# Performance work log

Hardware: AMD Instinct MI355X
Metric: run time of the kernel (lower is better)

## Reference

```python
import jax, jax.numpy as jnp
import numpy as np

B, S, D = 4, 2048, 1024

def setup_inputs() -> dict:
    key = jax.random.key(0)
    ks = jax.random.split(key, 7)
    sc = 1.0 / np.sqrt(D)
    return {
        "x": jax.random.normal(ks[0], (B, S, D), dtype=jnp.float32),
        "Wq": jax.random.normal(ks[1], (D, D), dtype=jnp.float32) * sc,
        "bq": jax.random.normal(ks[2], (D,), dtype=jnp.float32) * 0.01,
        "Wk": jax.random.normal(ks[3], (D, D), dtype=jnp.float32) * sc,
        "bk": jax.random.normal(ks[4], (D,), dtype=jnp.float32) * 0.01,
        "Wv": jax.random.normal(ks[5], (D, D), dtype=jnp.float32) * sc,
        "bv": jax.random.normal(ks[6], (D,), dtype=jnp.float32) * 0.01,
    }

def reference(x, Wq, bq, Wk, bk, Wv, bv):
    # q, k, v: [B, S, D] projections (torch Linear: x @ W^T + b; here W stored as [in, out])
    q = jnp.einsum("bsd,df->bsf", x, Wq) + bq
    k = jnp.einsum("bsd,df->bsf", x, Wk) + bk
    v = jnp.einsum("bsd,df->bsf", x, Wv) + bv
    dim = x.shape[-1]
    # scores: [B, S, S], scaled by sqrt(full d_model) as in the source
    scores = jnp.einsum("bqd,bkd->bqk", q, k) / jnp.sqrt(jnp.float32(dim)).astype(x.dtype)
    attn = jax.nn.softmax(scores, axis=-1)
    return jnp.einsum("bqk,bkd->bqd", attn, v)
```

## Files before the change

### kernel.cpp

```cpp
#include <hip/hip_runtime.h>
#include <hip/hip_bf16.h>

typedef __attribute__((ext_vector_type(8))) short bf16x8;
typedef __attribute__((ext_vector_type(4))) float f32x4;
typedef unsigned short u16;

__device__ __forceinline__ u16 f2bf(float f) {
  unsigned int u = __builtin_bit_cast(unsigned int, f);
  u += 0x7fffu + ((u >> 16) & 1u);
  return (u16)(u >> 16);
}
__device__ __forceinline__ float bf2f(unsigned int h) {
  unsigned int u = h << 16;
  return __builtin_bit_cast(float, u);
}

__device__ __forceinline__ void gload_lds16(const void* g, void* l) {
  __builtin_amdgcn_global_load_lds(
      (const __attribute__((address_space(1))) void*)g,
      (__attribute__((address_space(3))) void*)l, 16, 0, 0);
}

#define BAR() __builtin_amdgcn_s_barrier()
#define VMC(N) asm volatile("s_waitcnt vmcnt(%0)" ::"n"(N) : "memory")

template <int EPI>
__global__ __launch_bounds__(512, 2) void gemm2t(
    const u16* __restrict__ Abase, const u16* __restrict__ Btbase,
    const float* __restrict__ p0, float* __restrict__ p1,
    const float* __restrict__ p2, void* __restrict__ out0,
    void* __restrict__ out1, int Kd, int ldc, long long sAz, long long sBz,
    long long sCz) {
  constexpr int ASZ = 16384;
  constexpr int BSZ = 32768;
  constexpr int BBASE = 2 * ASZ;
  __shared__ char lds[2 * ASZ + 3 * BSZ];

  const int tid = threadIdx.x;
  const int w = tid >> 6, l = tid & 63;
  const int wr = w >> 2, wc = w & 3;
  const int lq = l >> 4, lr = l & 15;
  const int bm = blockIdx.y * 128, bn = blockIdx.x * 256;
  const int z = blockIdx.z;
  const u16* A = Abase + (size_t)z * sAz;
  const u16* Bt = Btbase + (size_t)z * sBz;
  const int NT = Kd >> 6;

  const int kbp = ((tid & 7) ^ ((tid >> 3) & 7)) * 8;
  const int drow = tid >> 3;
  const u16* gA[2];
  const u16* gB[4];
#pragma unroll
  for (int u = 0; u < 2; ++u)
    gA[u] = A + (size_t)(bm + u * 64 + drow) * Kd + kbp;
#pragma unroll
  for (int u = 0; u < 4; ++u)
    gB[u] = Bt + (size_t)(bn + u * 64 + drow) * Kd + kbp;

  auto stageA = [&](int kt) {
    char* d = lds + (kt & 1) * ASZ + tid * 16;
#pragma unroll
    for (int u = 0; u < 2; ++u) gload_lds16(gA[u] + kt * 64, d + u * 8192);
  };
  auto stageB = [&](int kt) {
    char* d = lds + BBASE + (kt % 3) * BSZ + tid * 16;
#pragma unroll
    for (int u = 0; u < 4; ++u) gload_lds16(gB[u] + kt * 64, d + u * 8192);
  };

  const int rA = wr * 64 + lr;
  const int rB0 = wc * 64 + lr;
  int aoff[2];
#pragma unroll
  for (int kh = 0; kh < 2; ++kh)
    aoff[kh] = rA * 128 + (((kh * 4 + lq) ^ (rA & 7)) << 4);

  f32x4 acc[4][2][2] = {};
  bf16x8 a[2][4];
  bf16x8 bb[2][2][2];

  auto rdA = [&](int kt) {
    const char* p = lds + (kt & 1) * ASZ;
#pragma unroll
    for (int kh = 0; kh < 2; ++kh)
#pragma unroll
      for (int mf = 0; mf < 4; ++mf)
        a[kh][mf] = *(const bf16x8*)(p + aoff[kh] + mf * 2048);
  };
  auto rdB = [&](int kt) {
    const char* p = lds + BBASE + (kt % 3) * BSZ;
#pragma unroll
    for (int nh = 0; nh < 2; ++nh) {
      const int rB = rB0 + nh * 32;
#pragma unroll
      for (int kh = 0; kh < 2; ++kh) {
        const int o = rB * 128 + (((kh * 4 + lq) ^ (rB & 7)) << 4);
#pragma unroll
        for (int nf = 0; nf < 2; ++nf)
          bb[nh][kh][nf] = *(const bf16x8*)(p + o + nf * 2048);
      }
    }
  };
  auto mma = [&](int kh) {
    __builtin_amdgcn_s_setprio(1);
#pragma unroll
    for (int nh = 0; nh < 2; ++nh)
#pragma unroll
      for (int mf = 0; mf < 4; ++mf)
#pragma unroll
        for (int nf = 0; nf < 2; ++nf)
          acc[mf][nh][nf] = __builtin_amdgcn_mfma_f32_16x16x32_bf16(
              a[kh][mf], bb[nh][kh][nf], acc[mf][nh][nf], 0, 0, 0);
    __builtin_amdgcn_s_setprio(0);
  };

  stageB(0);
  stageA(0);
  stageB(1);
  stageA(1);
  VMC(6);
  BAR();

  for (int t = 0; t < NT; ++t) {
    rdA(t);
    rdB(t);
    if (t + 2 < NT) stageB(t + 2);
    BAR();
    mma(0);
    if (t + 2 < NT) VMC(4); else VMC(0);
    BAR();
    if (t + 2 < NT) stageA(t + 2);
    mma(1);
  }

  if constexpr (EPI == 4) {
    constexpr float K2 = 0.045084834f;
    u16* C = (u16*)out0 + (size_t)z * sCz;
    const float* cc = p0 + z * 2048;
    float* rs = p1 + z * 2048;
    float psum[4][4] = {};
#pragma unroll
    for (int nh = 0; nh < 2; ++nh)
#pragma unroll
      for (int nf = 0; nf < 2; ++nf) {
        const int col = bn + wc * 64 + nh * 32 + nf * 16 + lr;
        const float cj2 = cc[col];
#pragma unroll
        for (int mf = 0; mf < 4; ++mf) {
          const int row = bm + wr * 64 + mf * 16 + lq * 4;
#pragma unroll
          for (int e = 0; e < 4; ++e) {
            const float pv = exp2f(fmaf(acc[mf][nh][nf][e], K2, cj2));
            C[(size_t)(row + e) * ldc + col] = f2bf(pv);
            psum[mf][e] += pv;
          }
        }
      }
#pragma unroll
    for (int off = 1; off <= 8; off <<= 1)
#pragma unroll
      for (int mf = 0; mf < 4; ++mf)
#pragma unroll
        for (int e = 0; e < 4; ++e)
          psum[mf][e] += __shfl_xor(psum[mf][e], off, 64);
    if (lr == 0) {
#pragma unroll
      for (int mf = 0; mf < 4; ++mf)
#pragma unroll
        for (int e = 0; e < 4; ++e)
          atomicAdd(&rs[bm + wr * 64 + mf * 16 + lq * 4 + e], psum[mf][e]);
    }
  } else if constexpr (EPI == 5) {
    float* C = (float*)out0 + (size_t)z * sCz;
    const float* rs = p1 + z * 2048;
#pragma unroll
    for (int nh = 0; nh < 2; ++nh)
#pragma unroll
      for (int nf = 0; nf < 2; ++nf) {
        const int col = bn + wc * 64 + nh * 32 + nf * 16 + lr;
#pragma unroll
        for (int mf = 0; mf < 4; ++mf) {
          const int row = bm + wr * 64 + mf * 16 + lq * 4;
#pragma unroll
          for (int e = 0; e < 4; ++e)
            C[(size_t)(row + e) * ldc + col] =
                acc[mf][nh][nf][e] / rs[row + e];
        }
      }
  } else {
    const int mat = bn >> 10;
    u16* T = (u16*)out0;
    u16* V = (u16*)out1;
#pragma unroll
    for (int nh = 0; nh < 2; ++nh)
#pragma unroll
      for (int nf = 0; nf < 2; ++nf) {
        const int oc = (bn + wc * 64 + nh * 32 + nf * 16 + lr) & 1023;
        if (mat == 0) {
#pragma unroll
          for (int mf = 0; mf < 4; ++mf) {
            const int row = bm + wr * 64 + mf * 16 + lq * 4;
#pragma unroll
            for (int e = 0; e < 4; ++e)
              T[(size_t)(row + e) * 1024 + oc] = f2bf(acc[mf][nh][nf][e]);
          }
        } else {
          const float bb2 = p2[oc];
#pragma unroll
          for (int mf = 0; mf < 4; ++mf) {
            const int row = bm + wr * 64 + mf * 16 + lq * 4;
            const int bz = row >> 11, sdx = row & 2047;
            ushort4 pk;
            pk.x = f2bf(acc[mf][nh][nf][0] + bb2);
            pk.y = f2bf(acc[mf][nh][nf][1] + bb2);
            pk.z = f2bf(acc[mf][nh][nf][2] + bb2);
            pk.w = f2bf(acc[mf][nh][nf][3] + bb2);
            *(ushort4*)&V[((size_t)bz * 1024 + oc) * 2048 + sdx] = pk;
          }
        }
      }
  }
}

__global__ __launch_bounds__(256) void gemmM(
    const u16* __restrict__ Abase, const u16* __restrict__ Btbase,
    float* __restrict__ out0, int Kd, int Kext, int ldc, long long sAz,
    long long sBz, long long sCz) {
  constexpr int ASZ = 16384;
  constexpr int BSZ = 16384;
  constexpr int BBASE = 2 * ASZ;
  __shared__ char lds[2 * ASZ + 3 * BSZ];

  const int tid = threadIdx.x;
  const int w = tid >> 6, l = tid & 63;
  const int wr = w >> 1, wc = w & 1;
  const int lq = l >> 4, lr = l & 15;
  const int bm = blockIdx.y * 128, bn = blockIdx.x * 128;
  const int z = blockIdx.z;
  const u16* A = Abase + (size_t)z * sAz;
  const u16* Bt = Btbase + (size_t)z * sBz;
  const int NT = Kext >> 6;

  const int kbp = ((tid & 7) ^ ((tid >> 3) & 7)) * 8;
  const int drow = tid >> 3;
  const u16* gA[4];
  const u16* gB[4];
#pragma unroll
  for (int u = 0; u < 4; ++u) {
    gA[u] = A + (size_t)(bm + u * 32 + drow) * Kd + kbp;
    gB[u] = Bt + (size_t)(bn + u * 32 + drow) * Kd + kbp;
  }

  auto stageA = [&](int kt) {
    char* d = lds + (kt & 1) * ASZ + tid * 16;
#pragma unroll
    for (int u = 0; u < 4; ++u) gload_lds16(gA[u] + kt * 64, d + u * 4096);
  };
  auto stageB = [&](int kt) {
    char* d = lds + BBASE + (kt % 3) * BSZ + tid * 16;
#pragma unroll
    for (int u = 0; u < 4; ++u) gload_lds16(gB[u] + kt * 64, d + u * 4096);
  };

  const int rA = wr * 64 + lr;
  const int rB0 = wc * 64 + lr;
  int aoff[2];
#pragma unroll
  for (int kh = 0; kh < 2; ++kh)
    aoff[kh] = rA * 128 + (((kh * 4 + lq) ^ (rA & 7)) << 4);

  f32x4 acc[4][2][2] = {};
  bf16x8 a[2][4];
  bf16x8 bb[2][2][2];

  auto rdA = [&](int kt) {
    const char* p = lds + (kt & 1) * ASZ;
#pragma unroll
    for (int kh = 0; kh < 2; ++kh)
#pragma unroll
      for (int mf = 0; mf < 4; ++mf)
        a[kh][mf] = *(const bf16x8*)(p + aoff[kh] + mf * 2048);
  };
  auto rdB = [&](int kt) {
    const char* p = lds + BBASE + (kt % 3) * BSZ;
#pragma unroll
    for (int nh = 0; nh < 2; ++nh) {
      const int rB = rB0 + nh * 32;
#pragma unroll
      for (int kh = 0; kh < 2; ++kh) {
        const int o = rB * 128 + (((kh * 4 + lq) ^ (rB & 7)) << 4);
#pragma unroll
        for (int nf = 0; nf < 2; ++nf)
          bb[nh][kh][nf] = *(const bf16x8*)(p + o + nf * 2048);
      }
    }
  };
  auto mma = [&](int kh) {
#pragma unroll
    for (int nh = 0; nh < 2; ++nh)
#pragma unroll
      for (int mf = 0; mf < 4; ++mf)
#pragma unroll
        for (int nf = 0; nf < 2; ++nf)
          acc[mf][nh][nf] = __builtin_amdgcn_mfma_f32_16x16x32_bf16(
              a[kh][mf], bb[nh][kh][nf], acc[mf][nh][nf], 0, 0, 0);
  };

  stageB(0);
  stageA(0);
  stageB(1);
  stageA(1);
  VMC(8);
  BAR();

  for (int t = 0; t < NT; ++t) {
    rdA(t);
    rdB(t);
    if (t + 2 < NT) stageB(t + 2);
    BAR();
    mma(0);
    if (t + 2 < NT) VMC(4); else VMC(0);
    BAR();
    if (t + 2 < NT) stageA(t + 2);
    mma(1);
  }

  float* C = out0 + (size_t)z * sCz;
#pragma unroll
  for (int nh = 0; nh < 2; ++nh)
#pragma unroll
    for (int nf = 0; nf < 2; ++nf) {
      const int col = bn + wc * 64 + nh * 32 + nf * 16 + lr;
#pragma unroll
      for (int mf = 0; mf < 4; ++mf) {
        const int row = bm + wr * 64 + mf * 16 + lq * 4;
#pragma unroll
        for (int e = 0; e < 4; ++e)
          C[(size_t)(row + e) * ldc + col] = acc[mf][nh][nf][e];
      }
    }
}

__global__ __launch_bounds__(256) void prep(
    const float* __restrict__ x, const float* __restrict__ Wq,
    const float* __restrict__ Wk, const float* __restrict__ Wv,
    const float* __restrict__ bq, u16* __restrict__ xb,
    u16* __restrict__ Wqb, u16* __restrict__ Wkb, u16* __restrict__ WtTV,
    float* __restrict__ vvec) {
  const int bid = blockIdx.x;
  const int tid = threadIdx.x;
  if (bid < 8192) {
    const int i = bid * 256 + tid;
    const float4 v = ((const float4*)x)[i];
    ushort4 o;
    o.x = f2bf(v.x);
    o.y = f2bf(v.y);
    o.z = f2bf(v.z);
    o.w = f2bf(v.w);
    ((ushort4*)xb)[i] = o;
  } else if (bid < 11264) {
    const int b = bid - 8192;
    const int zz = b >> 10, t2 = b & 1023;
    const int k0 = (t2 >> 5) * 32, n0 = (t2 & 31) * 32;
    const int tx = tid & 31, ty0 = tid >> 5;
    if (zz == 2) {
      __shared__ float s[32][33];
#pragma unroll
      for (int r = 0; r < 4; ++r) {
        const int row = ty0 + 8 * r;
        s[row][tx] = Wv[(size_t)(k0 + row) * 1024 + n0 + tx];
      }
      __syncthreads();
#pragma unroll
      for (int r = 0; r < 4; ++r) {
        const int row = ty0 + 8 * r;
        WtTV[1048576 + (size_t)(n0 + row) * 1024 + k0 + tx] =
            f2bf(s[tx][row]);
      }
    } else {
      const float* W = zz ? Wk : Wq;
      u16* O = zz ? Wkb : Wqb;
#pragma unroll
      for (int r = 0; r < 4; ++r) {
        const size_t i = (size_t)(k0 + ty0 + 8 * r) * 1024 + n0 + tx;
        O[i] = f2bf(W[i]);
      }
    }
  } else {
    const int d = bid - 11264;
    const float4 wv = ((const float4*)(Wk + (size_t)d * 1024))[tid];
    const float4 bv = ((const float4*)bq)[tid];
    float p = wv.x * bv.x + wv.y * bv.y + wv.z * bv.z + wv.w * bv.w;
#pragma unroll
    for (int o = 32; o; o >>= 1) p += __shfl_xor(p, o, 64);
    __shared__ float red[4];
    if ((tid & 63) == 0) red[tid >> 6] = p;
    __syncthreads();
    if (tid == 0) vvec[d] = red[0] + red[1] + red[2] + red[3];
  }
}

__global__ __launch_bounds__(256) void mcast(const float* __restrict__ Mf,
                                             u16* __restrict__ Mt) {
  const int i = blockIdx.x * 256 + threadIdx.x;
  const float4 a = ((const float4*)Mf)[i];
  const float4 b = ((const float4*)(Mf + 1048576))[i];
  const float4 c = ((const float4*)(Mf + 2097152))[i];
  const float4 d = ((const float4*)(Mf + 3145728))[i];
  ushort4 o;
  o.x = f2bf(a.x + b.x + c.x + d.x);
  o.y = f2bf(a.y + b.y + c.y + d.y);
  o.z = f2bf(a.z + b.z + c.z + d.z);
  o.w = f2bf(a.w + b.w + c.w + d.w);
  ((ushort4*)Mt)[i] = o;
}

__global__ __launch_bounds__(256) void cker(const u16* __restrict__ xb,
                                            const float* __restrict__ v,
                                            float* __restrict__ c,
                                            float* __restrict__ rowsum) {
  if (blockIdx.x < 32) rowsum[blockIdx.x * 256 + threadIdx.x] = 0.f;
  const int j = blockIdx.x * 8 + (threadIdx.x >> 5);
  const int lane = threadIdx.x & 31;
  const u16* xr = xb + (size_t)j * 1024;
  float p = 0.f;
#pragma unroll
  for (int k = 0; k < 4; ++k) {
    const int g = k * 32 + lane;
    const uint4 u = ((const uint4*)xr)[g];
    const float4 v0 = ((const float4*)v)[g * 2];
    const float4 v1 = ((const float4*)v)[g * 2 + 1];
    p += bf2f(u.x & 0xffffu) * v0.x + bf2f(u.x >> 16) * v0.y +
         bf2f(u.y & 0xffffu) * v0.z + bf2f(u.y >> 16) * v0.w +
         bf2f(u.z & 0xffffu) * v1.x + bf2f(u.z >> 16) * v1.y +
         bf2f(u.w & 0xffffu) * v1.z + bf2f(u.w >> 16) * v1.w;
  }
#pragma unroll
  for (int o = 16; o; o >>= 1) p += __shfl_xor(p, o, 64);
  if (lane == 0) c[j] = p * 0.045084834f;
}

extern "C" void kernel_launch(void* const* d_in, const int* in_sizes, int n_in,
                              void* d_out, int out_size, void* d_ws,
                              size_t ws_size, hipStream_t stream) {
  const float* x = (const float*)d_in[0];
  const float* Wq = (const float*)d_in[1];
  const float* bq = (const float*)d_in[2];
  const float* Wk = (const float*)d_in[3];
  const float* Wv = (const float*)d_in[5];
  const float* bv = (const float*)d_in[6];
  float* out = (float*)d_out;
  char* ws = (char*)d_ws;

  u16* xb = (u16*)ws;
  u16* WtTV = (u16*)(ws + 16777216);
  u16* Wqb = (u16*)(ws + 20971520);
  u16* Wkb = (u16*)(ws + 23068672);
  float* vvec = (float*)(ws + 25165824);
  float* cvec = (float*)(ws + 25169920);
  float* rowsum = (float*)(ws + 25202688);
  float* Mf32 = (float*)(ws + 25235456);
  u16* T = (u16*)(ws + 25235456);
  u16* Vt = (u16*)(ws + 42012672);
  u16* SP = (u16*)(ws + 58789888);

  prep<<<12288, 256, 0, stream>>>(x, Wq, Wk, Wv, bq, xb, Wqb, Wkb, WtTV,
                                  vvec);

  cker<<<1024, 256, 0, stream>>>(xb, vvec, cvec, rowsum);

  gemmM<<<dim3(8, 8, 4), 256, 0, stream>>>(Wkb, Wqb, Mf32, 1024, 256, 1024,
                                           256LL, 256LL, 1048576LL);
  mcast<<<1024, 256, 0, stream>>>(Mf32, WtTV);

  gemm2t<7><<<dim3(8, 64, 1), 512, 0, stream>>>(
      xb, WtTV, nullptr, nullptr, bv, T, Vt, 1024, 0, 0, 0, 0);

  gemm2t<4><<<dim3(8, 16, 4), 512, 0, stream>>>(
      T, xb, cvec, rowsum, nullptr, SP, nullptr, 1024, 2048, 2097152LL,
      2097152LL, 4194304LL);

  gemm2t<5><<<dim3(4, 16, 4), 512, 0, stream>>>(
      SP, Vt, nullptr, rowsum, nullptr, out, nullptr, 2048, 1024, 4194304LL,
      2097152LL, 2097152LL);
}
```

Baseline: 165.7 us.

## Remap GEMM workgroups per XCD and merge mcast with cker kernel

Each gemm2t workgroup's linear block ID is remapped so that consecutive tiles land on the same XCD. This is meant to improve L2 reuse of shared A/B tiles on the multi-die MI355X. Separately, the mcast (M reduction and bf16 cast) and cker (c vector and rowsum zeroing) kernels are fused into a single launch placed after gemmM, which removes one kernel launch. The cost is integer index arithmetic at each GEMM block start, and the cker work now runs after gemmM rather than before it.

```diff
diff --git a/kernel.cpp b/kernel.cpp
--- a/kernel.cpp
+++ b/kernel.cpp
@@ -36,12 +36,22 @@
   constexpr int BBASE = 2 * ASZ;
   __shared__ char lds[2 * ASZ + 3 * BSZ];
 
+  const int gx = gridDim.x, gy = gridDim.y;
+  const int nwg = gx * gy * gridDim.z;
+  const int orig = blockIdx.x + gx * (blockIdx.y + gy * blockIdx.z);
+  const int q = nwg >> 3, r = nwg & 7;
+  const int xcd = orig & 7, loc = orig >> 3;
+  const int wgid =
+      (xcd < r ? xcd * (q + 1) : r * (q + 1) + (xcd - r) * q) + loc;
+  const int bxi = wgid % gx;
+  const int byi = (wgid / gx) % gy;
+  const int z = wgid / (gx * gy);
+
   const int tid = threadIdx.x;
   const int w = tid >> 6, l = tid & 63;
   const int wr = w >> 2, wc = w & 3;
   const int lq = l >> 4, lr = l & 15;
-  const int bm = blockIdx.y * 128, bn = blockIdx.x * 256;
-  const int z = blockIdx.z;
+  const int bm = byi * 128, bn = bxi * 256;
   const u16* A = Abase + (size_t)z * sAz;
   const u16* Bt = Btbase + (size_t)z * sBz;
   const int NT = Kd >> 6;
@@ -400,44 +410,48 @@
   }
 }
 
-__global__ __launch_bounds__(256) void mcast(const float* __restrict__ Mf,
-                                             u16* __restrict__ Mt) {
-  const int i = blockIdx.x * 256 + threadIdx.x;
-  const float4 a = ((const float4*)Mf)[i];
-  const float4 b = ((const float4*)(Mf + 1048576))[i];
-  const float4 c = ((const float4*)(Mf + 2097152))[i];
-  const float4 d = ((const float4*)(Mf + 3145728))[i];
-  ushort4 o;
-  o.x = f2bf(a.x + b.x + c.x + d.x);
-  o.y = f2bf(a.y + b.y + c.y + d.y);
-  o.z = f2bf(a.z + b.z + c.z + d.z);
-  o.w = f2bf(a.w + b.w + c.w + d.w);
-  ((ushort4*)Mt)[i] = o;
-}
-
-__global__ __launch_bounds__(256) void cker(const u16* __restrict__ xb,
-                                            const float* __restrict__ v,
-                                            float* __restrict__ c,
-                                            float* __restrict__ rowsum) {
-  if (blockIdx.x < 32) rowsum[blockIdx.x * 256 + threadIdx.x] = 0.f;
-  const int j = blockIdx.x * 8 + (threadIdx.x >> 5);
-  const int lane = threadIdx.x & 31;
-  const u16* xr = xb + (size_t)j * 1024;
-  float p = 0.f;
-#pragma unroll
-  for (int k = 0; k < 4; ++k) {
-    const int g = k * 32 + lane;
-    const uint4 u = ((const uint4*)xr)[g];
-    const float4 v0 = ((const float4*)v)[g * 2];
-    const float4 v1 = ((const float4*)v)[g * 2 + 1];
-    p += bf2f(u.x & 0xffffu) * v0.x + bf2f(u.x >> 16) * v0.y +
-         bf2f(u.y & 0xffffu) * v0.z + bf2f(u.y >> 16) * v0.w +
-         bf2f(u.z & 0xffffu) * v1.x + bf2f(u.z >> 16) * v1.y +
-         bf2f(u.w & 0xffffu) * v1.z + bf2f(u.w >> 16) * v1.w;
-  }
-#pragma unroll
-  for (int o = 16; o; o >>= 1) p += __shfl_xor(p, o, 64);
-  if (lane == 0) c[j] = p * 0.045084834f;
+__global__ __launch_bounds__(256) void mck(const float* __restrict__ Mf,
+                                           u16* __restrict__ Mt,
+                                           const u16* __restrict__ xb,
+                                           const float* __restrict__ v,
+                                           float* __restrict__ c,
+                                           float* __restrict__ rowsum) {
+  const int bid = blockIdx.x;
+  const int tid = threadIdx.x;
+  if (bid < 1024) {
+    const int i = bid * 256 + tid;
+    const float4 a = ((const float4*)Mf)[i];
+    const float4 b = ((const float4*)(Mf + 1048576))[i];
+    const float4 cc = ((const float4*)(Mf + 2097152))[i];
+    const float4 d = ((const float4*)(Mf + 3145728))[i];
+    ushort4 o;
+    o.x = f2bf(a.x + b.x + cc.x + d.x);
+    o.y = f2bf(a.y + b.y + cc.y + d.y);
+    o.z = f2bf(a.z + b.z + cc.z + d.z);
+    o.w = f2bf(a.w + b.w + cc.w + d.w);
+    ((ushort4*)Mt)[i] = o;
+  } else {
+    const int b2 = bid - 1024;
+    if (b2 < 32) rowsum[b2 * 256 + tid] = 0.f;
+    const int j = b2 * 8 + (tid >> 5);
+    const int lane = tid & 31;
+    const u16* xr = xb + (size_t)j * 1024;
+    float p = 0.f;
+#pragma unroll
+    for (int k = 0; k < 4; ++k) {
+      const int g = k * 32 + lane;
+      const uint4 u = ((const uint4*)xr)[g];
+      const float4 v0 = ((const float4*)v)[g * 2];
+      const float4 v1 = ((const float4*)v)[g * 2 + 1];
+      p += bf2f(u.x & 0xffffu) * v0.x + bf2f(u.x >> 16) * v0.y +
+           bf2f(u.y & 0xffffu) * v0.z + bf2f(u.y >> 16) * v0.w +
+           bf2f(u.z & 0xffffu) * v1.x + bf2f(u.z >> 16) * v1.y +
+           bf2f(u.w & 0xffffu) * v1.z + bf2f(u.w >> 16) * v1.w;
+    }
+#pragma unroll
+    for (int o = 16; o; o >>= 1) p += __shfl_xor(p, o, 64);
+    if (lane == 0) c[j] = p * 0.045084834f;
+  }
 }
 
 extern "C" void kernel_launch(void* const* d_in, const int* in_sizes, int n_in,
@@ -467,11 +481,10 @@
   prep<<<12288, 256, 0, stream>>>(x, Wq, Wk, Wv, bq, xb, Wqb, Wkb, WtTV,
                                   vvec);
 
-  cker<<<1024, 256, 0, stream>>>(xb, vvec, cvec, rowsum);
-
   gemmM<<<dim3(8, 8, 4), 256, 0, stream>>>(Wkb, Wqb, Mf32, 1024, 256, 1024,
                                            256LL, 256LL, 1048576LL);
-  mcast<<<1024, 256, 0, stream>>>(Mf32, WtTV);
+
+  mck<<<2048, 256, 0, stream>>>(Mf32, WtTV, xb, vvec, cvec, rowsum);
 
   gemm2t<7><<<dim3(8, 64, 1), 512, 0, stream>>>(
       xb, WtTV, nullptr, nullptr, bv, T, Vt, 1024, 0, 0, 0, 0);
```

After: 164.7 us, median of 2. Within noise of the previous version (-0.6%).
